# Optimization experiments

Measured on AMD Instinct MI355X. Metric: run time of the kernel, lower is better.

## Reference

```python
import jax, jax.numpy as jnp
from jax import lax
import numpy as np

B, T, F, H = 256, 64, 256, 64  # batch, window_size, num_features, hidden (enc=dec)


def setup_inputs() -> dict:
    key = jax.random.key(0)
    ks = jax.random.split(key, 12)
    def n(k, shape, s=0.05):
        return jax.random.normal(k, shape, jnp.float32) * s
    return {
        "inputs": jax.random.normal(ks[0], (B, T, F), jnp.float32),
        # encoder LSTMCell (input = x_tilde of size F)
        "enc_kernel": n(ks[1], (F, 4 * H)),
        "enc_rec": n(ks[2], (H, 4 * H)),
        "enc_bias": jnp.zeros((4 * H,), jnp.float32),
        # decoder LSTMCell (input = y_tilde of size H)
        "dec_kernel": n(ks[3], (H, 4 * H)),
        "dec_rec": n(ks[4], (H, 4 * H)),
        "dec_bias": jnp.zeros((4 * H,), jnp.float32),
        # encoder attention: Dense(T, tanh) on [h;s;x_series] then Dense(1)
        "attn_e_W": n(ks[5], (2 * H + T, T)),
        "attn_e_b": jnp.zeros((T,), jnp.float32),
        "attn_e_v": n(ks[6], (T, 1)),
        "attn_e_vb": jnp.zeros((1,), jnp.float32),
        # decoder attention: Dense(H_enc, tanh) on [d;c;h_enc] then Dense(1)
        "attn_d_W": n(ks[7], (2 * H + H, H)),
        "attn_d_b": jnp.zeros((H,), jnp.float32),
        "attn_d_v": n(ks[8], (H, 1)),
        "attn_d_vb": jnp.zeros((1,), jnp.float32),
        # fc: (context H_enc + y_prev 1) -> H_dec
        "fc_W": n(ks[9], (H + 1, H)),
        "fc_b": jnp.zeros((H,), jnp.float32),
        # fc_final: (d_n H_dec + context H_enc) -> num_features
        "fcf_W": n(ks[10], (2 * H, F)),
        "fcf_b": jnp.zeros((F,), jnp.float32),
    }


def _lstm_step(x, h, c, K, R, b):
    # Keras LSTMCell gate order: i, f, g(candidate), o
    z = x @ K + h @ R + b
    i, f, g, o = jnp.split(z, 4, axis=-1)
    c_new = jax.nn.sigmoid(f) * c + jax.nn.sigmoid(i) * jnp.tanh(g)
    h_new = jax.nn.sigmoid(o) * jnp.tanh(c_new)
    return h_new, c_new


def _forward(inputs, enc_kernel, enc_rec, enc_bias, dec_kernel, dec_rec, dec_bias,
             attn_e_W, attn_e_b, attn_e_v, attn_e_vb,
             attn_d_W, attn_d_b, attn_d_v, attn_d_vb,
             fc_W, fc_b, fcf_W, fcf_b):
    Bn, Tn, Fn = inputs.shape
    Hn = enc_kernel.shape[1] // 4

    # ---------------- encoder (input attention over features) ----------------
    We_h, We_s, We_x = attn_e_W[:Hn], attn_e_W[Hn:2 * Hn], attn_e_W[2 * Hn:]
    x_series = jnp.transpose(inputs, (0, 2, 1))                 # (B, F, T): per-feature time series
    x_proj = jnp.einsum('bft,tu->bfu', x_series, We_x)          # (B, F, T), state-independent, hoisted

    def enc_step(carry, x_t):
        h, s = carry                                            # (B, H) each
        hs = h @ We_h + s @ We_s + attn_e_b                     # (B, T)
        e = jnp.tanh(hs[:, None, :] + x_proj)                   # (B, F, T)
        score = (e @ attn_e_v)[..., 0] + attn_e_vb              # (B, F)
        alpha = jax.nn.softmax(score, axis=1)                   # attention over features
        x_tilde = alpha * x_t                                   # (B, F)
        h2, s2 = _lstm_step(x_tilde, h, s, enc_kernel, enc_rec, enc_bias)
        return (h2, s2), h2

    z0 = jnp.zeros((Bn, Hn), inputs.dtype)
    _, h_all = lax.scan(enc_step, (z0, z0), jnp.transpose(inputs, (1, 0, 2)))
    x_encoded = jnp.transpose(h_all, (1, 0, 2))                 # (B, T, H)

    # ---------------- decoder (temporal attention over encoder states) ----------------
    Wd_d, Wd_c, Wd_x = attn_d_W[:Hn], attn_d_W[Hn:2 * Hn], attn_d_W[2 * Hn:]
    xe_proj = jnp.einsum('bte,eu->btu', x_encoded, Wd_x)        # (B, T, H), hoisted
    y_prev = inputs[:, :, -1]                                   # (B, T)

    def dec_step(carry, y_t):
        d, c = carry
        dc = d @ Wd_d + c @ Wd_c + attn_d_b                     # (B, H)
        e = jnp.tanh(dc[:, None, :] + xe_proj)                  # (B, T, H)
        score = (e @ attn_d_v)[..., 0] + attn_d_vb              # (B, T)
        beta = jax.nn.softmax(score, axis=1)                    # attention over time
        context = jnp.einsum('bt,bte->be', beta, x_encoded)     # (B, H)
        y_tilde = jnp.concatenate([context, y_t[:, None]], axis=1) @ fc_W + fc_b
        d2, c2 = _lstm_step(y_tilde, d, c, dec_kernel, dec_rec, dec_bias)
        return (d2, c2), context

    (d_n, _), ctxs = lax.scan(dec_step, (z0, z0), y_prev.T)
    context = ctxs[-1]                                          # context from last step
    y_pred = jnp.concatenate([d_n, context], axis=1) @ fcf_W + fcf_b  # (B, F)
    return y_pred[:, None, :]                                   # (B, 1, F)


def reference(inputs, enc_kernel, enc_rec, enc_bias, dec_kernel, dec_rec, dec_bias,
              attn_e_W, attn_e_b, attn_e_v, attn_e_vb,
              attn_d_W, attn_d_b, attn_d_v, attn_d_vb,
              fc_W, fc_b, fcf_W, fcf_b):
    return _forward(inputs, enc_kernel, enc_rec, enc_bias, dec_kernel, dec_rec, dec_bias,
                    attn_e_W, attn_e_b, attn_e_v, attn_e_vb,
                    attn_d_W, attn_d_b, attn_d_v, attn_d_vb,
                    fc_W, fc_b, fcf_W, fcf_b)
```

## Files before the change

kernel.cpp:

```cpp
#include <hip/hip_runtime.h>
#include <math.h>

#define ALIGN16 __attribute__((aligned(16)))

__device__ __forceinline__ float rcpf_(float x){ return __builtin_amdgcn_rcpf(x); }
__device__ __forceinline__ float tanh_e(float x){
  float t = __expf(2.0f*x);
  return (t - 1.0f) * rcpf_(t + 1.0f);
}
__device__ __forceinline__ float sigm(float x){
  return rcpf_(1.0f + __expf(-x));
}

__global__ __launch_bounds__(512)
void darnn_fused(const float* __restrict__ gin,
                 const float* __restrict__ eKg,
                 const float* __restrict__ eRg,
                 const float* __restrict__ ebg,
                 const float* __restrict__ dKg,
                 const float* __restrict__ dRg,
                 const float* __restrict__ dbg,
                 const float* __restrict__ aeW,
                 const float* __restrict__ aeb,
                 const float* __restrict__ aev,
                 const float* __restrict__ adW,
                 const float* __restrict__ adb,
                 const float* __restrict__ adv,
                 const float* __restrict__ fcW,
                 const float* __restrict__ fcb,
                 const float* __restrict__ fcfW,
                 const float* __restrict__ fcfb,
                 float* __restrict__ out)
{
  __shared__ ALIGN16 float sW[8256];
  __shared__ ALIGN16 float sWT[256*68];
  __shared__ ALIGN16 float s_xenc[64*65];
  __shared__ ALIGN16 float s_xtld[256];
  __shared__ ALIGN16 float s_ag[256];
  __shared__ ALIGN16 float s_hs[64];
  __shared__ ALIGN16 float s_h[64];
  __shared__ ALIGN16 float s_c[64];
  __shared__ ALIGN16 float s_aev[64];
  __shared__ ALIGN16 float s_pe[64];
  __shared__ ALIGN16 float s_ctx[64];
  __shared__ ALIGN16 float s_yprev[64];
  __shared__ ALIGN16 float s_redB[64];

  const int tid  = threadIdx.x;
  const int lane = tid & 63;
  const int wv   = tid >> 6;
  const int f    = tid >> 1;
  const int half = tid & 1;
  const int u8   = tid >> 3;
  const int grp  = tid & 7;
  const int b    = blockIdx.x;
  const float* inb = gin + (size_t)b * (64*256);

  for (int i = tid; i < 4096; i += 512) sW[i] = aeW[128*64 + i];
  if (tid < 64) { s_aev[tid] = aev[tid]; s_h[tid] = 0.f; s_c[tid] = 0.f; }
  __syncthreads();

  float P[32];
#pragma unroll
  for (int i = 0; i < 32; ++i) P[i] = 0.f;
  for (int t = 0; t < 64; ++t) {
    float xv = inb[t*256 + f];
#pragma unroll
    for (int q4 = 0; q4 < 8; ++q4) {
      float4 w = *(const float4*)&sW[t*64 + half*32 + q4*4];
      P[q4*4+0] = fmaf(xv, w.x, P[q4*4+0]);
      P[q4*4+1] = fmaf(xv, w.y, P[q4*4+1]);
      P[q4*4+2] = fmaf(xv, w.z, P[q4*4+2]);
      P[q4*4+3] = fmaf(xv, w.w, P[q4*4+3]);
    }
  }
#pragma unroll
  for (int i = 0; i < 32; ++i) P[i] = __expf(2.0f*P[i]);

  for (int i = tid; i < 16384; i += 512) sWT[(i & 255)*68 + (i >> 8)] = eRg[i];

  float eKr[128];
#pragma unroll
  for (int q = 0; q < 128; ++q) eKr[q] = eKg[(half*128 + q)*256 + f];
  float wh[8], wsr[8];
#pragma unroll
  for (int jj = 0; jj < 8; ++jj) {
    wh[jj]  = aeW[(grp*8+jj)*64 + u8];
    wsr[jj] = aeW[(64+grp*8+jj)*64 + u8];
  }
  const float aeb_u = aeb[u8];
  const float eb_k  = ebg[f];
  __syncthreads();

  for (int t = 0; t < 64; ++t) {
    float xtv = inb[t*256 + f];
    float4 h0 = *(const float4*)&s_h[grp*8];
    float4 h1 = *(const float4*)&s_h[grp*8+4];
    float4 c0 = *(const float4*)&s_c[grp*8];
    float4 c1 = *(const float4*)&s_c[grp*8+4];
    float p = 0.f;
    p = fmaf(h0.x, wh[0], p);  p = fmaf(h0.y, wh[1], p);
    p = fmaf(h0.z, wh[2], p);  p = fmaf(h0.w, wh[3], p);
    p = fmaf(h1.x, wh[4], p);  p = fmaf(h1.y, wh[5], p);
    p = fmaf(h1.z, wh[6], p);  p = fmaf(h1.w, wh[7], p);
    p = fmaf(c0.x, wsr[0], p); p = fmaf(c0.y, wsr[1], p);
    p = fmaf(c0.z, wsr[2], p); p = fmaf(c0.w, wsr[3], p);
    p = fmaf(c1.x, wsr[4], p); p = fmaf(c1.y, wsr[5], p);
    p = fmaf(c1.z, wsr[6], p); p = fmaf(c1.w, wsr[7], p);
    p += __shfl_xor(p, 1); p += __shfl_xor(p, 2); p += __shfl_xor(p, 4);
    float E = __expf(2.0f*(p + aeb_u));
    if (grp == 0) s_hs[u8] = E;
    __syncthreads();

    float sc = 0.f;
#pragma unroll
    for (int q4 = 0; q4 < 8; ++q4) {
      float4 Ev = *(const float4*)&s_hs[half*32 + q4*4];
      float4 vv = *(const float4*)&s_aev[half*32 + q4*4];
      float q0 = Ev.x*P[q4*4+0], q1 = Ev.y*P[q4*4+1];
      float q2 = Ev.z*P[q4*4+2], q3 = Ev.w*P[q4*4+3];
      sc = fmaf((q0-1.f)*rcpf_(q0+1.f), vv.x, sc);
      sc = fmaf((q1-1.f)*rcpf_(q1+1.f), vv.y, sc);
      sc = fmaf((q2-1.f)*rcpf_(q2+1.f), vv.z, sc);
      sc = fmaf((q3-1.f)*rcpf_(q3+1.f), vv.w, sc);
    }
    sc += __shfl_xor(sc, 1);
    float pe = __expf(sc);
    float ws = pe;
    ws += __shfl_xor(ws, 1);  ws += __shfl_xor(ws, 2);
    ws += __shfl_xor(ws, 4);  ws += __shfl_xor(ws, 8);
    ws += __shfl_xor(ws, 16); ws += __shfl_xor(ws, 32);
    if (lane == 0) s_redB[wv] = ws;
    if (half == 0) s_xtld[f] = pe * xtv;
    __syncthreads();

    float4 sA = *(const float4*)&s_redB[0];
    float4 sB = *(const float4*)&s_redB[4];
    float Sr = ((sA.x+sA.y)+(sA.z+sA.w)) + ((sB.x+sB.y)+(sB.z+sB.w));
    float invS = rcpf_(0.5f*Sr);
    float pa = 0.f;
#pragma unroll
    for (int q4 = 0; q4 < 32; ++q4) {
      float4 xt = *(const float4*)&s_xtld[half*128 + q4*4];
      pa = fmaf(xt.x, eKr[q4*4+0], pa);
      pa = fmaf(xt.y, eKr[q4*4+1], pa);
      pa = fmaf(xt.z, eKr[q4*4+2], pa);
      pa = fmaf(xt.w, eKr[q4*4+3], pa);
    }
    float ph = 0.f;
#pragma unroll
    for (int j4 = 0; j4 < 8; ++j4) {
      float4 hv = *(const float4*)&s_h[half*32 + j4*4];
      float4 w4 = *(const float4*)&sWT[f*68 + half*32 + j4*4];
      ph = fmaf(hv.x, w4.x, ph); ph = fmaf(hv.y, w4.y, ph);
      ph = fmaf(hv.z, w4.z, ph); ph = fmaf(hv.w, w4.w, ph);
    }
    float v = fmaf(pa, invS, ph);
    float z = v + __shfl_xor(v, 1) + eb_k;
    int gate = f >> 6;
    float a = (gate == 2) ? tanh_e(z) : sigm(z);
    if (half == 0) s_ag[f] = a;
    __syncthreads();

    if (tid < 64) {
      float cn = fmaf(s_ag[64+tid], s_c[tid], s_ag[tid]*s_ag[128+tid]);
      float hn = s_ag[192+tid]*tanh_e(cn);
      s_c[tid] = cn; s_h[tid] = hn; s_xenc[t*65 + tid] = hn;
    }
    __syncthreads();
  }

  for (int i = tid; i < 4096; i += 512) sW[i]        = adW[8192 + i];
  for (int i = tid; i < 4160; i += 512) sW[4096 + i] = fcW[i];
  if (tid < 64) { s_yprev[tid] = inb[tid*256 + 255]; s_h[tid] = 0.f; s_c[tid] = 0.f; }
  __syncthreads();

  float pd[8];
  {
    float xe[8];
#pragma unroll
    for (int q = 0; q < 8; ++q) xe[q] = 0.f;
    for (int e = 0; e < 64; ++e) {
      float xv = s_xenc[u8*65 + e];
      float4 w0 = *(const float4*)&sW[e*64 + grp*8];
      float4 w1 = *(const float4*)&sW[e*64 + grp*8 + 4];
      xe[0]=fmaf(xv,w0.x,xe[0]); xe[1]=fmaf(xv,w0.y,xe[1]);
      xe[2]=fmaf(xv,w0.z,xe[2]); xe[3]=fmaf(xv,w0.w,xe[3]);
      xe[4]=fmaf(xv,w1.x,xe[4]); xe[5]=fmaf(xv,w1.y,xe[5]);
      xe[6]=fmaf(xv,w1.z,xe[6]); xe[7]=fmaf(xv,w1.w,xe[7]);
    }
#pragma unroll
    for (int q = 0; q < 8; ++q) pd[q] = __expf(2.0f*xe[q]);
  }

  float macc[32];
#pragma unroll
  for (int i = 0; i < 32; ++i) macc[i] = 0.f;
  float m2k = 0.f, mbk = dbg[f];
  for (int j4 = 0; j4 < 16; ++j4) {
    float d0 = dKg[(j4*4+0)*256 + f];
    float d1 = dKg[(j4*4+1)*256 + f];
    float d2 = dKg[(j4*4+2)*256 + f];
    float d3 = dKg[(j4*4+3)*256 + f];
#pragma unroll
    for (int ii = 0; ii < 32; ++ii) {
      float4 w = *(const float4*)&sW[4096 + (half*32+ii)*64 + j4*4];
      macc[ii] = fmaf(w.x, d0, macc[ii]);
      macc[ii] = fmaf(w.y, d1, macc[ii]);
      macc[ii] = fmaf(w.z, d2, macc[ii]);
      macc[ii] = fmaf(w.w, d3, macc[ii]);
    }
    float4 wr = *(const float4*)&sW[4096 + 4096 + j4*4];
    m2k = fmaf(wr.x, d0, m2k); m2k = fmaf(wr.y, d1, m2k);
    m2k = fmaf(wr.z, d2, m2k); m2k = fmaf(wr.w, d3, m2k);
    mbk = fmaf(fcb[j4*4+0], d0, mbk); mbk = fmaf(fcb[j4*4+1], d1, mbk);
    mbk = fmaf(fcb[j4*4+2], d2, mbk); mbk = fmaf(fcb[j4*4+3], d3, mbk);
  }

  float dRr[32];
#pragma unroll
  for (int jj = 0; jj < 32; ++jj) dRr[jj] = dRg[(half*32+jj)*256 + f];
  float wdd[8], wdc[8], advr[8];
#pragma unroll
  for (int jj = 0; jj < 8; ++jj) {
    wdd[jj]  = adW[(grp*8+jj)*64 + u8];
    wdc[jj]  = adW[(64+grp*8+jj)*64 + u8];
    advr[jj] = adv[grp*8+jj];
  }
  const float adb_u = adb[u8];
  __syncthreads();

  for (int t = 0; t < 64; ++t) {
    float4 h0 = *(const float4*)&s_h[grp*8];
    float4 h1 = *(const float4*)&s_h[grp*8+4];
    float4 c0 = *(const float4*)&s_c[grp*8];
    float4 c1 = *(const float4*)&s_c[grp*8+4];
    float p = 0.f;
    p = fmaf(h0.x, wdd[0], p);  p = fmaf(h0.y, wdd[1], p);
    p = fmaf(h0.z, wdd[2], p);  p = fmaf(h0.w, wdd[3], p);
    p = fmaf(h1.x, wdd[4], p);  p = fmaf(h1.y, wdd[5], p);
    p = fmaf(h1.z, wdd[6], p);  p = fmaf(h1.w, wdd[7], p);
    p = fmaf(c0.x, wdc[0], p);  p = fmaf(c0.y, wdc[1], p);
    p = fmaf(c0.z, wdc[2], p);  p = fmaf(c0.w, wdc[3], p);
    p = fmaf(c1.x, wdc[4], p);  p = fmaf(c1.y, wdc[5], p);
    p = fmaf(c1.z, wdc[6], p);  p = fmaf(c1.w, wdc[7], p);
    p += __shfl_xor(p, 1); p += __shfl_xor(p, 2); p += __shfl_xor(p, 4);
    float E = __expf(2.0f*(p + adb_u));
    if (grp == 0) s_hs[u8] = E;
    __syncthreads();

    float4 E0 = *(const float4*)&s_hs[grp*8];
    float4 E1 = *(const float4*)&s_hs[grp*8+4];
    float sc = 0.f;
    {
      float q0=E0.x*pd[0], q1=E0.y*pd[1], q2=E0.z*pd[2], q3=E0.w*pd[3];
      float q4=E1.x*pd[4], q5=E1.y*pd[5], q6=E1.z*pd[6], q7=E1.w*pd[7];
      sc = fmaf((q0-1.f)*rcpf_(q0+1.f), advr[0], sc);
      sc = fmaf((q1-1.f)*rcpf_(q1+1.f), advr[1], sc);
      sc = fmaf((q2-1.f)*rcpf_(q2+1.f), advr[2], sc);
      sc = fmaf((q3-1.f)*rcpf_(q3+1.f), advr[3], sc);
      sc = fmaf((q4-1.f)*rcpf_(q4+1.f), advr[4], sc);
      sc = fmaf((q5-1.f)*rcpf_(q5+1.f), advr[5], sc);
      sc = fmaf((q6-1.f)*rcpf_(q6+1.f), advr[6], sc);
      sc = fmaf((q7-1.f)*rcpf_(q7+1.f), advr[7], sc);
    }
    sc += __shfl_xor(sc, 1); sc += __shfl_xor(sc, 2); sc += __shfl_xor(sc, 4);
    float pe = __expf(sc);
    float ws = pe;
    ws += __shfl_xor(ws, 1);  ws += __shfl_xor(ws, 2);
    ws += __shfl_xor(ws, 4);  ws += __shfl_xor(ws, 8);
    ws += __shfl_xor(ws, 16); ws += __shfl_xor(ws, 32);
    if (lane == 0) s_redB[wv] = ws;
    if (grp == 0) s_pe[u8] = pe;
    __syncthreads();

    float4 sA = *(const float4*)&s_redB[0];
    float4 sB = *(const float4*)&s_redB[4];
    float Sr = ((sA.x+sA.y)+(sA.z+sA.w)) + ((sB.x+sB.y)+(sB.z+sB.w));
    float invS = rcpf_(0.125f*Sr);
    float pc = 0.f;
#pragma unroll
    for (int q = 0; q < 8; ++q)
      pc = fmaf(s_pe[grp*8+q], s_xenc[(grp*8+q)*65 + u8], pc);
    pc += __shfl_xor(pc, 1); pc += __shfl_xor(pc, 2); pc += __shfl_xor(pc, 4);
    float ce = pc * invS;
    if (grp == 0) s_ctx[u8] = ce;
    __syncthreads();

    float pa = 0.f;
#pragma unroll
    for (int i4 = 0; i4 < 8; ++i4) {
      float4 cv = *(const float4*)&s_ctx[half*32 + i4*4];
      pa = fmaf(cv.x, macc[i4*4+0], pa);
      pa = fmaf(cv.y, macc[i4*4+1], pa);
      pa = fmaf(cv.z, macc[i4*4+2], pa);
      pa = fmaf(cv.w, macc[i4*4+3], pa);
    }
#pragma unroll
    for (int j4 = 0; j4 < 8; ++j4) {
      float4 hv = *(const float4*)&s_h[half*32 + j4*4];
      pa = fmaf(hv.x, dRr[j4*4+0], pa);
      pa = fmaf(hv.y, dRr[j4*4+1], pa);
      pa = fmaf(hv.z, dRr[j4*4+2], pa);
      pa = fmaf(hv.w, dRr[j4*4+3], pa);
    }
    float y_t = s_yprev[t];
    if (half == 0) pa = fmaf(y_t, m2k, pa + mbk);
    float z = pa + __shfl_xor(pa, 1);
    int gate = f >> 6;
    float a = (gate == 2) ? tanh_e(z) : sigm(z);
    if (half == 0) s_ag[f] = a;
    __syncthreads();

    if (tid < 64) {
      float cn = fmaf(s_ag[64+tid], s_c[tid], s_ag[tid]*s_ag[128+tid]);
      s_c[tid] = cn;
      s_h[tid] = s_ag[192+tid]*tanh_e(cn);
    }
    __syncthreads();
  }

  {
    const float* src = half ? s_ctx : s_h;
    float pa = 0.f;
#pragma unroll
    for (int j4 = 0; j4 < 16; ++j4) {
      float4 v = *(const float4*)&src[j4*4];
      pa = fmaf(v.x, fcfW[(half*64 + j4*4+0)*256 + f], pa);
      pa = fmaf(v.y, fcfW[(half*64 + j4*4+1)*256 + f], pa);
      pa = fmaf(v.z, fcfW[(half*64 + j4*4+2)*256 + f], pa);
      pa = fmaf(v.w, fcfW[(half*64 + j4*4+3)*256 + f], pa);
    }
    float r = pa + __shfl_xor(pa, 1);
    if (half == 0) out[b*256 + f] = r + fcfb[f];
  }
}

extern "C" void kernel_launch(void* const* d_in, const int* in_sizes, int n_in,
                              void* d_out, int out_size, void* d_ws, size_t ws_size,
                              hipStream_t stream) {
  const float* gin  = (const float*)d_in[0];
  const float* eK   = (const float*)d_in[1];
  const float* eR   = (const float*)d_in[2];
  const float* eb   = (const float*)d_in[3];
  const float* dK   = (const float*)d_in[4];
  const float* dR   = (const float*)d_in[5];
  const float* db   = (const float*)d_in[6];
  const float* aeW  = (const float*)d_in[7];
  const float* aeb  = (const float*)d_in[8];
  const float* aev  = (const float*)d_in[9];
  const float* adW  = (const float*)d_in[11];
  const float* adb  = (const float*)d_in[12];
  const float* adv  = (const float*)d_in[13];
  const float* fcW  = (const float*)d_in[15];
  const float* fcb  = (const float*)d_in[16];
  const float* fcfW = (const float*)d_in[17];
  const float* fcfb = (const float*)d_in[18];
  float* out = (float*)d_out;

  const int B = in_sizes[0] / (64*256);
  hipLaunchKernelGGL(darnn_fused, dim3(B), dim3(512), 0, stream,
                     gin, eK, eR, eb, dK, dR, db, aeW, aeb, aev,
                     adW, adb, adv, fcW, fcb, fcfW, fcfb, out);
}
```

Measured before the change: 444.7 us.

## Double block to 1024 threads and restructure encoder/decoder recurrences

Raises the per-batch block from 512 to 1024 threads, splitting each gate's dot products four ways instead of two so per-thread register arrays shrink (eKr goes from 128 to 64 entries). The h/c state update is now done redundantly in every wave and carried in registers, with shuffles replacing shared-memory reads of c. This removes one barrier per timestep. The decoder precomputes the context-to-gate projection over all timesteps (x_enc·fcW·dK) into shared memory, so each step only needs a softmax-weighted sum. The trade-off is more threads per reduction, redundant gate math across waves, and higher shared-memory use (about 140KB), which likely caps occupancy at one block per CU.

Result: slower. 1.124 ms (+152.8%).

```diff
diff --git a/kernel.cpp b/kernel.cpp
--- a/kernel.cpp
+++ b/kernel.cpp
@@ -12,7 +12,7 @@
   return rcpf_(1.0f + __expf(-x));
 }
 
-__global__ __launch_bounds__(512)
+__global__ __launch_bounds__(1024, 4)
 void darnn_fused(const float* __restrict__ gin,
                  const float* __restrict__ eKg,
                  const float* __restrict__ eRg,
@@ -32,307 +32,332 @@
                  const float* __restrict__ fcfb,
                  float* __restrict__ out)
 {
-  __shared__ ALIGN16 float sW[8256];
-  __shared__ ALIGN16 float sWT[256*68];
-  __shared__ ALIGN16 float s_xenc[64*65];
+  __shared__ ALIGN16 float s_buf[17408];
+  __shared__ ALIGN16 float s_wx2[17408];
+  __shared__ ALIGN16 float s_xenc[64*68];
+  __shared__ ALIGN16 float s_ag[256];
   __shared__ ALIGN16 float s_xtld[256];
-  __shared__ ALIGN16 float s_ag[256];
   __shared__ ALIGN16 float s_hs[64];
-  __shared__ ALIGN16 float s_h[64];
-  __shared__ ALIGN16 float s_c[64];
-  __shared__ ALIGN16 float s_aev[64];
   __shared__ ALIGN16 float s_pe[64];
+  __shared__ ALIGN16 float s_redB[16];
   __shared__ ALIGN16 float s_ctx[64];
   __shared__ ALIGN16 float s_yprev[64];
-  __shared__ ALIGN16 float s_redB[64];
+  __shared__ ALIGN16 float s_fcb[64];
+  __shared__ ALIGN16 float s_h[64];
+  __shared__ ALIGN16 float s_aev[64];
 
   const int tid  = threadIdx.x;
   const int lane = tid & 63;
   const int wv   = tid >> 6;
-  const int f    = tid >> 1;
-  const int half = tid & 1;
-  const int u8   = tid >> 3;
-  const int grp  = tid & 7;
+  const int u    = tid >> 4;
+  const int g16  = tid & 15;
+  const int f    = tid >> 2;
+  const int q4   = tid & 3;
   const int b    = blockIdx.x;
   const float* inb = gin + (size_t)b * (64*256);
 
-  for (int i = tid; i < 4096; i += 512) sW[i] = aeW[128*64 + i];
-  if (tid < 64) { s_aev[tid] = aev[tid]; s_h[tid] = 0.f; s_c[tid] = 0.f; }
-  __syncthreads();
-
-  float P[32];
-#pragma unroll
-  for (int i = 0; i < 32; ++i) P[i] = 0.f;
-  for (int t = 0; t < 64; ++t) {
-    float xv = inb[t*256 + f];
-#pragma unroll
-    for (int q4 = 0; q4 < 8; ++q4) {
-      float4 w = *(const float4*)&sW[t*64 + half*32 + q4*4];
-      P[q4*4+0] = fmaf(xv, w.x, P[q4*4+0]);
-      P[q4*4+1] = fmaf(xv, w.y, P[q4*4+1]);
-      P[q4*4+2] = fmaf(xv, w.z, P[q4*4+2]);
-      P[q4*4+3] = fmaf(xv, w.w, P[q4*4+3]);
-    }
-  }
-#pragma unroll
-  for (int i = 0; i < 32; ++i) P[i] = __expf(2.0f*P[i]);
-
-  for (int i = tid; i < 16384; i += 512) sWT[(i & 255)*68 + (i >> 8)] = eRg[i];
-
-  float eKr[128];
-#pragma unroll
-  for (int q = 0; q < 128; ++q) eKr[q] = eKg[(half*128 + q)*256 + f];
-  float wh[8], wsr[8];
-#pragma unroll
-  for (int jj = 0; jj < 8; ++jj) {
-    wh[jj]  = aeW[(grp*8+jj)*64 + u8];
-    wsr[jj] = aeW[(64+grp*8+jj)*64 + u8];
-  }
-  const float aeb_u = aeb[u8];
+  for (int i = tid; i < 4096; i += 1024) s_buf[i] = aeW[8192 + i];
+  if (tid < 64) { s_aev[tid] = aev[tid]; s_h[tid] = 0.f; }
+  __syncthreads();
+
+  float P[16];
+  {
+    float xp[16];
+#pragma unroll
+    for (int i = 0; i < 16; ++i) xp[i] = 0.f;
+    for (int t = 0; t < 64; ++t) {
+      float xv = inb[t*256 + f];
+#pragma unroll
+      for (int i4 = 0; i4 < 4; ++i4) {
+        float4 w = *(const float4*)&s_buf[t*64 + q4*16 + i4*4];
+        xp[i4*4+0] = fmaf(xv, w.x, xp[i4*4+0]);
+        xp[i4*4+1] = fmaf(xv, w.y, xp[i4*4+1]);
+        xp[i4*4+2] = fmaf(xv, w.z, xp[i4*4+2]);
+        xp[i4*4+3] = fmaf(xv, w.w, xp[i4*4+3]);
+      }
+    }
+#pragma unroll
+    for (int i = 0; i < 16; ++i) P[i] = __expf(2.0f*xp[i]);
+  }
+  __syncthreads();
+
+  for (int i = tid; i < 16384; i += 1024)
+    s_buf[(i >> 8)*257 + (i & 255)] = eRg[i];
+
+  float eKr[64];
+#pragma unroll
+  for (int ff = 0; ff < 64; ++ff) eKr[ff] = eKg[(q4*64 + ff)*256 + f];
+
+  float wh[4], wsr[4];
+#pragma unroll
+  for (int jj = 0; jj < 4; ++jj) {
+    wh[jj]  = aeW[(g16*4 + jj)*64 + u];
+    wsr[jj] = aeW[(64 + g16*4 + jj)*64 + u];
+  }
+  const float aeb_u = aeb[u];
   const float eb_k  = ebg[f];
+  float h_j = 0.f, c_j = 0.f;
   __syncthreads();
 
   for (int t = 0; t < 64; ++t) {
     float xtv = inb[t*256 + f];
-    float4 h0 = *(const float4*)&s_h[grp*8];
-    float4 h1 = *(const float4*)&s_h[grp*8+4];
-    float4 c0 = *(const float4*)&s_c[grp*8];
-    float4 c1 = *(const float4*)&s_c[grp*8+4];
+    if (t > 0) {
+      float gi = s_ag[lane], gf = s_ag[64+lane], gg = s_ag[128+lane], go = s_ag[192+lane];
+      c_j = fmaf(gf, c_j, gi*gg);
+      h_j = go * tanh_e(c_j);
+      if (wv == 0) { s_h[lane] = h_j; s_xenc[(t-1)*68 + lane] = h_j; }
+    }
     float p = 0.f;
-    p = fmaf(h0.x, wh[0], p);  p = fmaf(h0.y, wh[1], p);
-    p = fmaf(h0.z, wh[2], p);  p = fmaf(h0.w, wh[3], p);
-    p = fmaf(h1.x, wh[4], p);  p = fmaf(h1.y, wh[5], p);
-    p = fmaf(h1.z, wh[6], p);  p = fmaf(h1.w, wh[7], p);
-    p = fmaf(c0.x, wsr[0], p); p = fmaf(c0.y, wsr[1], p);
-    p = fmaf(c0.z, wsr[2], p); p = fmaf(c0.w, wsr[3], p);
-    p = fmaf(c1.x, wsr[4], p); p = fmaf(c1.y, wsr[5], p);
-    p = fmaf(c1.z, wsr[6], p); p = fmaf(c1.w, wsr[7], p);
-    p += __shfl_xor(p, 1); p += __shfl_xor(p, 2); p += __shfl_xor(p, 4);
+#pragma unroll
+    for (int jj = 0; jj < 4; ++jj) {
+      float hh = __shfl(h_j, g16*4 + jj);
+      float cc = __shfl(c_j, g16*4 + jj);
+      p = fmaf(hh, wh[jj], p);
+      p = fmaf(cc, wsr[jj], p);
+    }
+    p += __shfl_xor(p,1); p += __shfl_xor(p,2); p += __shfl_xor(p,4); p += __shfl_xor(p,8);
     float E = __expf(2.0f*(p + aeb_u));
-    if (grp == 0) s_hs[u8] = E;
+    if (g16 == 0) s_hs[u] = E;
     __syncthreads();
 
     float sc = 0.f;
 #pragma unroll
-    for (int q4 = 0; q4 < 8; ++q4) {
-      float4 Ev = *(const float4*)&s_hs[half*32 + q4*4];
-      float4 vv = *(const float4*)&s_aev[half*32 + q4*4];
-      float q0 = Ev.x*P[q4*4+0], q1 = Ev.y*P[q4*4+1];
-      float q2 = Ev.z*P[q4*4+2], q3 = Ev.w*P[q4*4+3];
-      sc = fmaf((q0-1.f)*rcpf_(q0+1.f), vv.x, sc);
-      sc = fmaf((q1-1.f)*rcpf_(q1+1.f), vv.y, sc);
-      sc = fmaf((q2-1.f)*rcpf_(q2+1.f), vv.z, sc);
-      sc = fmaf((q3-1.f)*rcpf_(q3+1.f), vv.w, sc);
-    }
-    sc += __shfl_xor(sc, 1);
+    for (int i4 = 0; i4 < 4; ++i4) {
+      float4 Ev = *(const float4*)&s_hs[q4*16 + i4*4];
+      float4 vv = *(const float4*)&s_aev[q4*16 + i4*4];
+      float w0 = Ev.x*P[i4*4+0], w1 = Ev.y*P[i4*4+1];
+      float w2 = Ev.z*P[i4*4+2], w3 = Ev.w*P[i4*4+3];
+      sc = fmaf((w0-1.f)*rcpf_(w0+1.f), vv.x, sc);
+      sc = fmaf((w1-1.f)*rcpf_(w1+1.f), vv.y, sc);
+      sc = fmaf((w2-1.f)*rcpf_(w2+1.f), vv.z, sc);
+      sc = fmaf((w3-1.f)*rcpf_(w3+1.f), vv.w, sc);
+    }
+    sc += __shfl_xor(sc,1); sc += __shfl_xor(sc,2);
     float pe = __expf(sc);
     float ws = pe;
-    ws += __shfl_xor(ws, 1);  ws += __shfl_xor(ws, 2);
-    ws += __shfl_xor(ws, 4);  ws += __shfl_xor(ws, 8);
-    ws += __shfl_xor(ws, 16); ws += __shfl_xor(ws, 32);
+    ws += __shfl_xor(ws,4);  ws += __shfl_xor(ws,8);
+    ws += __shfl_xor(ws,16); ws += __shfl_xor(ws,32);
     if (lane == 0) s_redB[wv] = ws;
-    if (half == 0) s_xtld[f] = pe * xtv;
-    __syncthreads();
-
-    float4 sA = *(const float4*)&s_redB[0];
-    float4 sB = *(const float4*)&s_redB[4];
-    float Sr = ((sA.x+sA.y)+(sA.z+sA.w)) + ((sB.x+sB.y)+(sB.z+sB.w));
-    float invS = rcpf_(0.5f*Sr);
+    if (q4 == 0) s_xtld[f] = pe * xtv;
+    __syncthreads();
+
+    float4 r0 = *(const float4*)&s_redB[0];
+    float4 r1 = *(const float4*)&s_redB[4];
+    float4 r2 = *(const float4*)&s_redB[8];
+    float4 r3 = *(const float4*)&s_redB[12];
+    float S = ((r0.x+r0.y)+(r0.z+r0.w)) + ((r1.x+r1.y)+(r1.z+r1.w))
+            + ((r2.x+r2.y)+(r2.z+r2.w)) + ((r3.x+r3.y)+(r3.z+r3.w));
+    float invS = rcpf_(S);
     float pa = 0.f;
 #pragma unroll
-    for (int q4 = 0; q4 < 32; ++q4) {
-      float4 xt = *(const float4*)&s_xtld[half*128 + q4*4];
-      pa = fmaf(xt.x, eKr[q4*4+0], pa);
-      pa = fmaf(xt.y, eKr[q4*4+1], pa);
-      pa = fmaf(xt.z, eKr[q4*4+2], pa);
-      pa = fmaf(xt.w, eKr[q4*4+3], pa);
+    for (int f4 = 0; f4 < 16; ++f4) {
+      float4 xt = *(const float4*)&s_xtld[q4*64 + f4*4];
+      pa = fmaf(xt.x, eKr[f4*4+0], pa);
+      pa = fmaf(xt.y, eKr[f4*4+1], pa);
+      pa = fmaf(xt.z, eKr[f4*4+2], pa);
+      pa = fmaf(xt.w, eKr[f4*4+3], pa);
     }
     float ph = 0.f;
 #pragma unroll
-    for (int j4 = 0; j4 < 8; ++j4) {
-      float4 hv = *(const float4*)&s_h[half*32 + j4*4];
-      float4 w4 = *(const float4*)&sWT[f*68 + half*32 + j4*4];
-      ph = fmaf(hv.x, w4.x, ph); ph = fmaf(hv.y, w4.y, ph);
-      ph = fmaf(hv.z, w4.z, ph); ph = fmaf(hv.w, w4.w, ph);
+    for (int j4 = 0; j4 < 4; ++j4) {
+      float4 hv = *(const float4*)&s_h[q4*16 + j4*4];
+      ph = fmaf(hv.x, s_buf[(q4*16 + j4*4+0)*257 + f], ph);
+      ph = fmaf(hv.y, s_buf[(q4*16 + j4*4+1)*257 + f], ph);
+      ph = fmaf(hv.z, s_buf[(q4*16 + j4*4+2)*257 + f], ph);
+      ph = fmaf(hv.w, s_buf[(q4*16 + j4*4+3)*257 + f], ph);
     }
     float v = fmaf(pa, invS, ph);
-    float z = v + __shfl_xor(v, 1) + eb_k;
-    int gate = f >> 6;
-    float a = (gate == 2) ? tanh_e(z) : sigm(z);
-    if (half == 0) s_ag[f] = a;
-    __syncthreads();
-
-    if (tid < 64) {
-      float cn = fmaf(s_ag[64+tid], s_c[tid], s_ag[tid]*s_ag[128+tid]);
-      float hn = s_ag[192+tid]*tanh_e(cn);
-      s_c[tid] = cn; s_h[tid] = hn; s_xenc[t*65 + tid] = hn;
-    }
-    __syncthreads();
-  }
-
-  for (int i = tid; i < 4096; i += 512) sW[i]        = adW[8192 + i];
-  for (int i = tid; i < 4160; i += 512) sW[4096 + i] = fcW[i];
-  if (tid < 64) { s_yprev[tid] = inb[tid*256 + 255]; s_h[tid] = 0.f; s_c[tid] = 0.f; }
-  __syncthreads();
-
-  float pd[8];
-  {
-    float xe[8];
-#pragma unroll
-    for (int q = 0; q < 8; ++q) xe[q] = 0.f;
+    v += __shfl_xor(v,1); v += __shfl_xor(v,2);
+    v += eb_k;
+    float a = ((f >> 6) == 2) ? tanh_e(v) : sigm(v);
+    if (q4 == 0) s_ag[f] = a;
+    __syncthreads();
+  }
+  {
+    float gi = s_ag[lane], gf = s_ag[64+lane], gg = s_ag[128+lane], go = s_ag[192+lane];
+    c_j = fmaf(gf, c_j, gi*gg);
+    h_j = go * tanh_e(c_j);
+    if (wv == 0) s_xenc[63*68 + lane] = h_j;
+  }
+
+  h_j = 0.f; c_j = 0.f;
+  if (tid < 64) { s_h[tid] = 0.f; s_yprev[tid] = inb[tid*256 + 255]; s_fcb[tid] = fcb[tid]; }
+  for (int i = tid; i < 4096; i += 1024) s_wx2[i] = adW[8192 + i];
+  __syncthreads();
+
+  float pd_[4];
+  {
+    float xe0 = 0.f, xe1 = 0.f, xe2 = 0.f, xe3 = 0.f;
     for (int e = 0; e < 64; ++e) {
-      float xv = s_xenc[u8*65 + e];
-      float4 w0 = *(const float4*)&sW[e*64 + grp*8];
-      float4 w1 = *(const float4*)&sW[e*64 + grp*8 + 4];
-      xe[0]=fmaf(xv,w0.x,xe[0]); xe[1]=fmaf(xv,w0.y,xe[1]);
-      xe[2]=fmaf(xv,w0.z,xe[2]); xe[3]=fmaf(xv,w0.w,xe[3]);
-      xe[4]=fmaf(xv,w1.x,xe[4]); xe[5]=fmaf(xv,w1.y,xe[5]);
-      xe[6]=fmaf(xv,w1.z,xe[6]); xe[7]=fmaf(xv,w1.w,xe[7]);
-    }
-#pragma unroll
-    for (int q = 0; q < 8; ++q) pd[q] = __expf(2.0f*xe[q]);
-  }
-
-  float macc[32];
-#pragma unroll
-  for (int i = 0; i < 32; ++i) macc[i] = 0.f;
+      float xv = s_xenc[u*68 + e];
+      float4 w = *(const float4*)&s_wx2[e*64 + g16*4];
+      xe0 = fmaf(xv, w.x, xe0);
+      xe1 = fmaf(xv, w.y, xe1);
+      xe2 = fmaf(xv, w.z, xe2);
+      xe3 = fmaf(xv, w.w, xe3);
+    }
+    pd_[0] = __expf(2.0f*xe0); pd_[1] = __expf(2.0f*xe1);
+    pd_[2] = __expf(2.0f*xe2); pd_[3] = __expf(2.0f*xe3);
+  }
+  float dKr[64];
+#pragma unroll
+  for (int j = 0; j < 64; ++j) dKr[j] = dKg[j*256 + f];
+  float wdd[4], wdc[4], advr[4];
+#pragma unroll
+  for (int jj = 0; jj < 4; ++jj) {
+    wdd[jj]  = adW[(g16*4 + jj)*64 + u];
+    wdc[jj]  = adW[(64 + g16*4 + jj)*64 + u];
+    advr[jj] = adv[g16*4 + jj];
+  }
+  const float adb_u = adb[u];
+  __syncthreads();
+  for (int i = tid; i < 4160; i += 1024) s_wx2[i] = fcW[i];
+  __syncthreads();
+
+  for (int ee = 0; ee < 16; ++ee) {
+    int e = q4*16 + ee;
+    float acc = 0.f;
+#pragma unroll
+    for (int j4 = 0; j4 < 16; ++j4) {
+      float4 w = *(const float4*)&s_wx2[e*64 + j4*4];
+      acc = fmaf(w.x, dKr[j4*4+0], acc);
+      acc = fmaf(w.y, dKr[j4*4+1], acc);
+      acc = fmaf(w.z, dKr[j4*4+2], acc);
+      acc = fmaf(w.w, dKr[j4*4+3], acc);
+    }
+    s_buf[f*68 + e] = acc;
+  }
   float m2k = 0.f, mbk = dbg[f];
+#pragma unroll
   for (int j4 = 0; j4 < 16; ++j4) {
-    float d0 = dKg[(j4*4+0)*256 + f];
-    float d1 = dKg[(j4*4+1)*256 + f];
-    float d2 = dKg[(j4*4+2)*256 + f];
-    float d3 = dKg[(j4*4+3)*256 + f];
-#pragma unroll
-    for (int ii = 0; ii < 32; ++ii) {
-      float4 w = *(const float4*)&sW[4096 + (half*32+ii)*64 + j4*4];
-      macc[ii] = fmaf(w.x, d0, macc[ii]);
-      macc[ii] = fmaf(w.y, d1, macc[ii]);
-      macc[ii] = fmaf(w.z, d2, macc[ii]);
-      macc[ii] = fmaf(w.w, d3, macc[ii]);
-    }
-    float4 wr = *(const float4*)&sW[4096 + 4096 + j4*4];
-    m2k = fmaf(wr.x, d0, m2k); m2k = fmaf(wr.y, d1, m2k);
-    m2k = fmaf(wr.z, d2, m2k); m2k = fmaf(wr.w, d3, m2k);
-    mbk = fmaf(fcb[j4*4+0], d0, mbk); mbk = fmaf(fcb[j4*4+1], d1, mbk);
-    mbk = fmaf(fcb[j4*4+2], d2, mbk); mbk = fmaf(fcb[j4*4+3], d3, mbk);
-  }
-
-  float dRr[32];
-#pragma unroll
-  for (int jj = 0; jj < 32; ++jj) dRr[jj] = dRg[(half*32+jj)*256 + f];
-  float wdd[8], wdc[8], advr[8];
-#pragma unroll
-  for (int jj = 0; jj < 8; ++jj) {
-    wdd[jj]  = adW[(grp*8+jj)*64 + u8];
-    wdc[jj]  = adW[(64+grp*8+jj)*64 + u8];
-    advr[jj] = adv[grp*8+jj];
-  }
-  const float adb_u = adb[u8];
-  __syncthreads();
+    float4 w  = *(const float4*)&s_wx2[4096 + j4*4];
+    float4 fb = *(const float4*)&s_fcb[j4*4];
+    m2k = fmaf(w.x,  dKr[j4*4+0], m2k); m2k = fmaf(w.y,  dKr[j4*4+1], m2k);
+    m2k = fmaf(w.z,  dKr[j4*4+2], m2k); m2k = fmaf(w.w,  dKr[j4*4+3], m2k);
+    mbk = fmaf(fb.x, dKr[j4*4+0], mbk); mbk = fmaf(fb.y, dKr[j4*4+1], mbk);
+    mbk = fmaf(fb.z, dKr[j4*4+2], mbk); mbk = fmaf(fb.w, dKr[j4*4+3], mbk);
+  }
+  __syncthreads();
+
+  for (int tt = 0; tt < 16; ++tt) {
+    int t = q4*16 + tt;
+    float acc = 0.f;
+#pragma unroll
+    for (int e4 = 0; e4 < 16; ++e4) {
+      float4 xv = *(const float4*)&s_xenc[t*68 + e4*4];
+      float4 mv = *(const float4*)&s_buf[f*68 + e4*4];
+      acc = fmaf(xv.x, mv.x, acc); acc = fmaf(xv.y, mv.y, acc);
+      acc = fmaf(xv.z, mv.z, acc); acc = fmaf(xv.w, mv.w, acc);
+    }
+    s_wx2[f*68 + t] = acc;
+  }
+  __syncthreads();
+
+  for (int i = tid; i < 16384; i += 1024)
+    s_buf[(i >> 8)*257 + (i & 255)] = dRg[i];
 
   for (int t = 0; t < 64; ++t) {
-    float4 h0 = *(const float4*)&s_h[grp*8];
-    float4 h1 = *(const float4*)&s_h[grp*8+4];
-    float4 c0 = *(const float4*)&s_c[grp*8];
-    float4 c1 = *(const float4*)&s_c[grp*8+4];
+    if (t > 0) {
+      float gi = s_ag[lane], gf = s_ag[64+lane], gg = s_ag[128+lane], go = s_ag[192+lane];
+      c_j = fmaf(gf, c_j, gi*gg);
+      h_j = go * tanh_e(c_j);
+      if (wv == 0) s_h[lane] = h_j;
+    }
     float p = 0.f;
-    p = fmaf(h0.x, wdd[0], p);  p = fmaf(h0.y, wdd[1], p);
-    p = fmaf(h0.z, wdd[2], p);  p = fmaf(h0.w, wdd[3], p);
-    p = fmaf(h1.x, wdd[4], p);  p = fmaf(h1.y, wdd[5], p);
-    p = fmaf(h1.z, wdd[6], p);  p = fmaf(h1.w, wdd[7], p);
-    p = fmaf(c0.x, wdc[0], p);  p = fmaf(c0.y, wdc[1], p);
-    p = fmaf(c0.z, wdc[2], p);  p = fmaf(c0.w, wdc[3], p);
-    p = fmaf(c1.x, wdc[4], p);  p = fmaf(c1.y, wdc[5], p);
-    p = fmaf(c1.z, wdc[6], p);  p = fmaf(c1.w, wdc[7], p);
-    p += __shfl_xor(p, 1); p += __shfl_xor(p, 2); p += __shfl_xor(p, 4);
+#pragma unroll
+    for (int jj = 0; jj < 4; ++jj) {
+      float hh = __shfl(h_j, g16*4 + jj);
+      float cc = __shfl(c_j, g16*4 + jj);
+      p = fmaf(hh, wdd[jj], p);
+      p = fmaf(cc, wdc[jj], p);
+    }
+    p += __shfl_xor(p,1); p += __shfl_xor(p,2); p += __shfl_xor(p,4); p += __shfl_xor(p,8);
     float E = __expf(2.0f*(p + adb_u));
-    if (grp == 0) s_hs[u8] = E;
-    __syncthreads();
-
-    float4 E0 = *(const float4*)&s_hs[grp*8];
-    float4 E1 = *(const float4*)&s_hs[grp*8+4];
-    float sc = 0.f;
-    {
-      float q0=E0.x*pd[0], q1=E0.y*pd[1], q2=E0.z*pd[2], q3=E0.w*pd[3];
-      float q4=E1.x*pd[4], q5=E1.y*pd[5], q6=E1.z*pd[6], q7=E1.w*pd[7];
-      sc = fmaf((q0-1.f)*rcpf_(q0+1.f), advr[0], sc);
-      sc = fmaf((q1-1.f)*rcpf_(q1+1.f), advr[1], sc);
-      sc = fmaf((q2-1.f)*rcpf_(q2+1.f), advr[2], sc);
-      sc = fmaf((q3-1.f)*rcpf_(q3+1.f), advr[3], sc);
-      sc = fmaf((q4-1.f)*rcpf_(q4+1.f), advr[4], sc);
-      sc = fmaf((q5-1.f)*rcpf_(q5+1.f), advr[5], sc);
-      sc = fmaf((q6-1.f)*rcpf_(q6+1.f), advr[6], sc);
-      sc = fmaf((q7-1.f)*rcpf_(q7+1.f), advr[7], sc);
-    }
-    sc += __shfl_xor(sc, 1); sc += __shfl_xor(sc, 2); sc += __shfl_xor(sc, 4);
+    if (g16 == 0) s_hs[u] = E;
+    __syncthreads();
+
+    float4 Ev = *(const float4*)&s_hs[g16*4];
+    float w0 = Ev.x*pd_[0], w1 = Ev.y*pd_[1], w2 = Ev.z*pd_[2], w3 = Ev.w*pd_[3];
+    float sc =        (w0-1.f)*rcpf_(w0+1.f) * advr[0];
+    sc = fmaf((w1-1.f)*rcpf_(w1+1.f), advr[1], sc);
+    sc = fmaf((w2-1.f)*rcpf_(w2+1.f), advr[2], sc);
+    sc = fmaf((w3-1.f)*rcpf_(w3+1.f), advr[3], sc);
+    sc += __shfl_xor(sc,1); sc += __shfl_xor(sc,2); sc += __shfl_xor(sc,4); sc += __shfl_xor(sc,8);
     float pe = __expf(sc);
+    if (g16 == 0) s_pe[u] = pe;
     float ws = pe;
-    ws += __shfl_xor(ws, 1);  ws += __shfl_xor(ws, 2);
-    ws += __shfl_xor(ws, 4);  ws += __shfl_xor(ws, 8);
-    ws += __shfl_xor(ws, 16); ws += __shfl_xor(ws, 32);
+    ws += __shfl_xor(ws,16); ws += __shfl_xor(ws,32);
     if (lane == 0) s_redB[wv] = ws;
-    if (grp == 0) s_pe[u8] = pe;
-    __syncthreads();
-
-    float4 sA = *(const float4*)&s_redB[0];
-    float4 sB = *(const float4*)&s_redB[4];
-    float Sr = ((sA.x+sA.y)+(sA.z+sA.w)) + ((sB.x+sB.y)+(sB.z+sB.w));
-    float invS = rcpf_(0.125f*Sr);
+    __syncthreads();
+
+    float4 r0 = *(const float4*)&s_redB[0];
+    float4 r1 = *(const float4*)&s_redB[4];
+    float4 r2 = *(const float4*)&s_redB[8];
+    float4 r3 = *(const float4*)&s_redB[12];
+    float S = ((r0.x+r0.y)+(r0.z+r0.w)) + ((r1.x+r1.y)+(r1.z+r1.w))
+            + ((r2.x+r2.y)+(r2.z+r2.w)) + ((r3.x+r3.y)+(r3.z+r3.w));
+    float invS = rcpf_(S);
+    float pa1 = 0.f;
+#pragma unroll
+    for (int t4 = 0; t4 < 4; ++t4) {
+      float4 pv = *(const float4*)&s_pe[q4*16 + t4*4];
+      float4 xm = *(const float4*)&s_wx2[f*68 + q4*16 + t4*4];
+      pa1 = fmaf(pv.x, xm.x, pa1); pa1 = fmaf(pv.y, xm.y, pa1);
+      pa1 = fmaf(pv.z, xm.z, pa1); pa1 = fmaf(pv.w, xm.w, pa1);
+    }
+    float pa2 = 0.f;
+#pragma unroll
+    for (int j4 = 0; j4 < 4; ++j4) {
+      float4 hv = *(const float4*)&s_h[q4*16 + j4*4];
+      pa2 = fmaf(hv.x, s_buf[(q4*16 + j4*4+0)*257 + f], pa2);
+      pa2 = fmaf(hv.y, s_buf[(q4*16 + j4*4+1)*257 + f], pa2);
+      pa2 = fmaf(hv.z, s_buf[(q4*16 + j4*4+2)*257 + f], pa2);
+      pa2 = fmaf(hv.w, s_buf[(q4*16 + j4*4+3)*257 + f], pa2);
+    }
+    float v = fmaf(pa1, invS, pa2);
+    if (q4 == 0) v = fmaf(s_yprev[t], m2k, v + mbk);
+    v += __shfl_xor(v,1); v += __shfl_xor(v,2);
+    float a = ((f >> 6) == 2) ? tanh_e(v) : sigm(v);
+    if (q4 == 0) s_ag[f] = a;
+    __syncthreads();
+  }
+  {
+    float gi = s_ag[lane], gf = s_ag[64+lane], gg = s_ag[128+lane], go = s_ag[192+lane];
+    c_j = fmaf(gf, c_j, gi*gg);
+    h_j = go * tanh_e(c_j);
+    if (wv == 0) s_h[lane] = h_j;
+  }
+  {
+    float4 r0 = *(const float4*)&s_redB[0];
+    float4 r1 = *(const float4*)&s_redB[4];
+    float4 r2 = *(const float4*)&s_redB[8];
+    float4 r3 = *(const float4*)&s_redB[12];
+    float S = ((r0.x+r0.y)+(r0.z+r0.w)) + ((r1.x+r1.y)+(r1.z+r1.w))
+            + ((r2.x+r2.y)+(r2.z+r2.w)) + ((r3.x+r3.y)+(r3.z+r3.w));
+    float invS = rcpf_(S);
     float pc = 0.f;
 #pragma unroll
-    for (int q = 0; q < 8; ++q)
-      pc = fmaf(s_pe[grp*8+q], s_xenc[(grp*8+q)*65 + u8], pc);
-    pc += __shfl_xor(pc, 1); pc += __shfl_xor(pc, 2); pc += __shfl_xor(pc, 4);
-    float ce = pc * invS;
-    if (grp == 0) s_ctx[u8] = ce;
-    __syncthreads();
-
+    for (int tt = 0; tt < 4; ++tt)
+      pc = fmaf(s_pe[g16*4 + tt], s_xenc[(g16*4 + tt)*68 + u], pc);
+    pc += __shfl_xor(pc,1); pc += __shfl_xor(pc,2); pc += __shfl_xor(pc,4); pc += __shfl_xor(pc,8);
+    if (g16 == 0) s_ctx[u] = pc * invS;
+  }
+  __syncthreads();
+
+  {
+    const float* src = (q4 < 2) ? &s_h[q4*32] : &s_ctx[(q4-2)*32];
     float pa = 0.f;
 #pragma unroll
     for (int i4 = 0; i4 < 8; ++i4) {
-      float4 cv = *(const float4*)&s_ctx[half*32 + i4*4];
-      pa = fmaf(cv.x, macc[i4*4+0], pa);
-      pa = fmaf(cv.y, macc[i4*4+1], pa);
-      pa = fmaf(cv.z, macc[i4*4+2], pa);
-      pa = fmaf(cv.w, macc[i4*4+3], pa);
-    }
-#pragma unroll
-    for (int j4 = 0; j4 < 8; ++j4) {
-      float4 hv = *(const float4*)&s_h[half*32 + j4*4];
-      pa = fmaf(hv.x, dRr[j4*4+0], pa);
-      pa = fmaf(hv.y, dRr[j4*4+1], pa);
-      pa = fmaf(hv.z, dRr[j4*4+2], pa);
-      pa = fmaf(hv.w, dRr[j4*4+3], pa);
-    }
-    float y_t = s_yprev[t];
-    if (half == 0) pa = fmaf(y_t, m2k, pa + mbk);
-    float z = pa + __shfl_xor(pa, 1);
-    int gate = f >> 6;
-    float a = (gate == 2) ? tanh_e(z) : sigm(z);
-    if (half == 0) s_ag[f] = a;
-    __syncthreads();
-
-    if (tid < 64) {
-      float cn = fmaf(s_ag[64+tid], s_c[tid], s_ag[tid]*s_ag[128+tid]);
-      s_c[tid] = cn;
-      s_h[tid] = s_ag[192+tid]*tanh_e(cn);
-    }
-    __syncthreads();
-  }
-
-  {
-    const float* src = half ? s_ctx : s_h;
-    float pa = 0.f;
-#pragma unroll
-    for (int j4 = 0; j4 < 16; ++j4) {
-      float4 v = *(const float4*)&src[j4*4];
-      pa = fmaf(v.x, fcfW[(half*64 + j4*4+0)*256 + f], pa);
-      pa = fmaf(v.y, fcfW[(half*64 + j4*4+1)*256 + f], pa);
-      pa = fmaf(v.z, fcfW[(half*64 + j4*4+2)*256 + f], pa);
-      pa = fmaf(v.w, fcfW[(half*64 + j4*4+3)*256 + f], pa);
-    }
-    float r = pa + __shfl_xor(pa, 1);
-    if (half == 0) out[b*256 + f] = r + fcfb[f];
+      float4 vv = *(const float4*)&src[i4*4];
+      int row = q4*32 + i4*4;
+      pa = fmaf(vv.x, fcfW[(row+0)*256 + f], pa);
+      pa = fmaf(vv.y, fcfW[(row+1)*256 + f], pa);
+      pa = fmaf(vv.z, fcfW[(row+2)*256 + f], pa);
+      pa = fmaf(vv.w, fcfW[(row+3)*256 + f], pa);
+    }
+    pa += __shfl_xor(pa,1); pa += __shfl_xor(pa,2);
+    if (q4 == 0) out[b*256 + f] = pa + fcfb[f];
   }
 }
 
@@ -359,7 +384,7 @@
   float* out = (float*)d_out;
 
   const int B = in_sizes[0] / (64*256);
-  hipLaunchKernelGGL(darnn_fused, dim3(B), dim3(512), 0, stream,
+  hipLaunchKernelGGL(darnn_fused, dim3(B), dim3(1024), 0, stream,
                      gin, eK, eR, eb, dK, dR, db, aeW, aeb, aev,
                      adW, adb, adv, fcW, fcb, fcfW, fcfb, out);
 }
```
